# Kernel tuning notes

Hardware: AMD Instinct MI355X
Metric: run time of the kernel (lower is better)

## Reference

```python
import jax, jax.numpy as jnp
import numpy as np

IN_F = 128
OUT_F = 128
GROUPS = 8
NUM_F = 8
B = 16
NP_ = 4096


def setup_inputs() -> dict:
    key = jax.random.key(0)
    ks = jax.random.split(key, 6)
    x = jax.random.normal(ks[0], (B, NP_, IN_F), dtype=jnp.float32)
    grid = jnp.arange(NUM_F, dtype=jnp.float32) + 1.0                      # [num_f]
    base_weight = jax.random.normal(ks[1], (OUT_F, IN_F), dtype=jnp.float32) * 0.05
    scale_sp = jnp.ones((OUT_F,), dtype=jnp.float32)
    coef = jax.random.uniform(ks[2], (GROUPS, 1, NUM_F), dtype=jnp.float32)
    conv_w = jax.random.normal(ks[3], (NUM_F, OUT_F, IN_F), dtype=jnp.float32) * 0.05  # grouped 1x1 conv
    conv_b = jax.random.normal(ks[4], (NUM_F, OUT_F), dtype=jnp.float32) * 0.05
    return {"x": x, "grid": grid, "base_weight": base_weight,
            "scale_sp": scale_sp, "coef": coef, "conv_w": conv_w, "conv_b": conv_b}


def reference(x, grid, base_weight, scale_sp, coef, conv_w, conv_b):
    Bd, Nd, D = x.shape
    num_f = grid.shape[0]
    groups = coef.shape[0]
    gsz = D // groups
    xf = x.reshape(Bd * Nd, D)                                  # [batch, in]
    # base path: SiLU then linear (no bias)
    base = jax.nn.silu(xf) @ base_weight.T                       # [batch, out]
    # spline path: sin(grid * x), broadcast coef per (group, f)
    s = jnp.sin(grid[None, :, None] * xf[:, None, :])            # [batch, num_f, in]
    cm = coef[:, 0, :].T                                         # [num_f, groups]
    s = s.reshape(-1, num_f, groups, gsz) * cm[None, :, :, None]
    s = s.reshape(-1, num_f, D)                                  # [batch, num_f, in]
    # grouped 1x1 conv == per-f GEMM
    spline = jnp.einsum('bfi,foi->bfo', s, conv_w) + conv_b[None]
    spline = spline.sum(axis=1) * scale_sp                       # [batch, out]
    out = (base + spline).reshape(Bd, Nd, -1)
    return out
```

## Files before the change

### kernel.cpp

```cpp
#include <hip/hip_runtime.h>
#include <hip/hip_bf16.h>
#include <stdint.h>

#define IN_F   128
#define OUT_F  128
#define NUM_F  8
#define NROWS  (16*4096)

typedef __bf16  bf16x8  __attribute__((ext_vector_type(8)));
typedef float   f32x16  __attribute__((ext_vector_type(16)));
typedef float   f32x4   __attribute__((ext_vector_type(4)));

#define WP_CHUNKS (8*9*4*64)
#define SBLK      36864

__device__ __attribute__((aligned(256))) __bf16 g_Wp[WP_CHUNKS * 8];
__device__ float  g_bias[OUT_F];

__global__ __launch_bounds__(256) void skan_prep(
    const float* __restrict__ base_w,
    const float* __restrict__ scale,
    const float* __restrict__ coef,
    const float* __restrict__ conv_w,
    const float* __restrict__ conv_b)
{
    int gid = blockIdx.x * 256 + threadIdx.x;
    int l  = gid & 63;
    int t  = (gid >> 6) & 3;
    int r  = gid >> 8;
    int s  = r / 9;
    int fb = r % 9;
    int n  = t * 32 + (l & 31);
    int k0 = s * 16 + (l >> 5) * 8;
    __bf16* dst = g_Wp + (size_t)gid * 8;
    if (fb == 0) {
        #pragma unroll
        for (int j = 0; j < 8; ++j)
            dst[j] = (__bf16)base_w[n * IN_F + k0 + j];
    } else {
        int f = fb - 1;
        float sc = scale[n];
        #pragma unroll
        for (int j = 0; j < 8; ++j) {
            int k = k0 + j;
            float v = conv_w[((size_t)f * OUT_F + n) * IN_F + k]
                      * coef[(k >> 4) * NUM_F + f] * sc;
            dst[j] = (__bf16)v;
        }
    }
    if (gid < OUT_F) {
        float b = 0.f;
        #pragma unroll
        for (int f = 0; f < NUM_F; ++f) b += conv_b[f * OUT_F + gid];
        g_bias[gid] = b * scale[gid];
    }
}

__device__ __forceinline__ void gld_lds16(const void* g, void* l) {
    __builtin_amdgcn_global_load_lds(
        (const __attribute__((address_space(1))) uint32_t*)g,
        (__attribute__((address_space(3))) uint32_t*)l, 16, 0, 0);
}

__global__ __launch_bounds__(256, 2) void skan_main(
    const float* __restrict__ x,
    float* __restrict__ out)
{
    __shared__ uint4 smem4[4608];
    char* smem = (char*)smem4;

    const int tid = threadIdx.x;
    const int w   = tid >> 6;
    const int l   = tid & 63;
    const int hl  = l & 31;
    const int h   = l >> 5;
    const int m0  = blockIdx.x * 128 + w * 32;
    const int m   = m0 + hl;

    const char* wpb = (const char*)g_Wp;

    #pragma unroll
    for (int r = 0; r < 9; ++r)
        gld_lds16(wpb + (r * 256 + tid) * 16, smem + (r * 256 + tid) * 16);
    asm volatile("" ::: "memory");

    const f32x4* x4 = (const f32x4*)x + (size_t)m * (IN_F / 4) + 2 * h;
    f32x4 xa[8], xb[8];
    xa[0] = x4[0]; xb[0] = x4[1];
    xa[1] = x4[4]; xb[1] = x4[5];

    f32x16 acc[4];
    #pragma unroll
    for (int t = 0; t < 4; ++t)
        #pragma unroll
        for (int r = 0; r < 16; ++r) acc[t][r] = 0.f;

    #pragma unroll
    for (int s = 0; s < 8; ++s) {
        if (s < 7) asm volatile("s_waitcnt vmcnt(2)" ::: "memory");
        else       asm volatile("s_waitcnt vmcnt(0)" ::: "memory");
        __builtin_amdgcn_s_barrier();

        if (s < 7) {
            const char* src = wpb + (size_t)(s + 1) * SBLK;
            char*       dst = smem + ((s + 1) & 1) * SBLK;
            #pragma unroll
            for (int r = 0; r < 9; ++r)
                gld_lds16(src + (r * 256 + tid) * 16, dst + (r * 256 + tid) * 16);
        }
        asm volatile("" ::: "memory");
        if (s < 6) { xa[s + 2] = x4[4 * (s + 2)]; xb[s + 2] = x4[4 * (s + 2) + 1]; }

        bf16x8 af[9];
        #pragma unroll
        for (int j = 0; j < 8; ++j) {
            float v = (j < 4) ? xa[s][j] : xb[s][j - 4];
            float sv = v * __builtin_amdgcn_rcpf(1.0f + __expf(-v));
            af[0][j] = (__bf16)sv;
            float u  = __builtin_amdgcn_fractf(v * 0.15915494309189535f);
            float s1 = __builtin_amdgcn_sinf(u);
            float c2 = 2.0f * __builtin_amdgcn_cosf(u);
            af[1][j] = (__bf16)s1;
            float sp = s1;
            float sc = c2 * s1;
            af[2][j] = (__bf16)sc;
            #pragma unroll
            for (int f = 3; f <= 8; ++f) {
                float sn = c2 * sc - sp;
                af[f][j] = (__bf16)sn;
                sp = sc; sc = sn;
            }
        }

        const bf16x8* bp = (const bf16x8*)(smem + (s & 1) * SBLK);
        #pragma unroll
        for (int fb = 0; fb < 9; ++fb)
            #pragma unroll
            for (int t = 0; t < 4; ++t) {
                bf16x8 b = bp[(fb * 4 + t) * 64 + l];
                acc[t] = __builtin_amdgcn_mfma_f32_32x32x16_bf16(af[fb], b, acc[t], 0, 0, 0);
            }
    }

    #pragma unroll
    for (int t = 0; t < 4; ++t) {
        float bv = g_bias[t * 32 + hl];
        #pragma unroll
        for (int r = 0; r < 16; ++r) {
            int row = (r & 3) + 8 * (r >> 2) + 4 * h;
            out[(size_t)(m0 + row) * OUT_F + t * 32 + hl] = acc[t][r] + bv;
        }
    }
}

extern "C" void kernel_launch(void* const* d_in, const int* in_sizes, int n_in,
                              void* d_out, int out_size, void* d_ws, size_t ws_size,
                              hipStream_t stream) {
    const float* x      = (const float*)d_in[0];
    const float* base_w = (const float*)d_in[2];
    const float* scale  = (const float*)d_in[3];
    const float* coef   = (const float*)d_in[4];
    const float* conv_w = (const float*)d_in[5];
    const float* conv_b = (const float*)d_in[6];
    float* out = (float*)d_out;
    (void)d_ws; (void)ws_size;

    skan_prep<<<WP_CHUNKS / 256, 256, 0, stream>>>(base_w, scale, coef, conv_w, conv_b);
    skan_main<<<NROWS / 128, 256, 0, stream>>>(x, out);
}
```

Measured before the change: 109.0 us.

## Retile waves to 64x64 output blocks and double-buffer x loads

Each wave now computes a 64-row by 64-column output tile (2x2 MFMA tiles) instead of 32 rows by all 128 columns. It therefore loads only half of each B stage from LDS, and each B fragment feeds two MFMAs. In exchange, each wave computes silu/sin features for twice as many rows. Because the two column-half waves of a row pair compute identical features, the transcendental work per block doubles. The x prefetch is reduced to a two-slot ring issued after the feature computation, with the vmcnt wait adjusted to match.

Result: no change. 110.4 us (+1.3%).

```diff
diff --git a/kernel.cpp b/kernel.cpp
--- a/kernel.cpp
+++ b/kernel.cpp
@@ -62,6 +62,24 @@
         (__attribute__((address_space(3))) uint32_t*)l, 16, 0, 0);
 }
 
+__device__ __forceinline__ void skan_af(float v, bf16x8* af, int j) {
+    float sv = v * __builtin_amdgcn_rcpf(1.0f + __expf(-v));
+    af[0][j] = (__bf16)sv;
+    float u  = __builtin_amdgcn_fractf(v * 0.15915494309189535f);
+    float s1 = __builtin_amdgcn_sinf(u);
+    float c2 = 2.0f * __builtin_amdgcn_cosf(u);
+    af[1][j] = (__bf16)s1;
+    float sp = s1;
+    float sc = c2 * s1;
+    af[2][j] = (__bf16)sc;
+    #pragma unroll
+    for (int f = 3; f <= 8; ++f) {
+        float sn = c2 * sc - sp;
+        af[f][j] = (__bf16)sn;
+        sp = sc; sc = sn;
+    }
+}
+
 __global__ __launch_bounds__(256, 2) void skan_main(
     const float* __restrict__ x,
     float* __restrict__ out)
@@ -74,8 +92,10 @@
     const int l   = tid & 63;
     const int hl  = l & 31;
     const int h   = l >> 5;
-    const int m0  = blockIdx.x * 128 + w * 32;
-    const int m   = m0 + hl;
+    const int rw  = w >> 1;
+    const int cw  = w & 1;
+    const int mlo = blockIdx.x * 128 + rw * 64 + hl;
+    const int mhi = mlo + 32;
 
     const char* wpb = (const char*)g_Wp;
 
@@ -84,10 +104,11 @@
         gld_lds16(wpb + (r * 256 + tid) * 16, smem + (r * 256 + tid) * 16);
     asm volatile("" ::: "memory");
 
-    const f32x4* x4 = (const f32x4*)x + (size_t)m * (IN_F / 4) + 2 * h;
-    f32x4 xa[8], xb[8];
-    xa[0] = x4[0]; xb[0] = x4[1];
-    xa[1] = x4[4]; xb[1] = x4[5];
+    const f32x4* xLo = (const f32x4*)x + (size_t)mlo * (IN_F / 4) + 2 * h;
+    const f32x4* xHi = (const f32x4*)x + (size_t)mhi * (IN_F / 4) + 2 * h;
+    f32x4 xal[2], xbl[2], xah[2], xbh[2];
+    xal[0] = xLo[0]; xbl[0] = xLo[1]; xah[0] = xHi[0]; xbh[0] = xHi[1];
+    xal[1] = xLo[4]; xbl[1] = xLo[5]; xah[1] = xHi[4]; xbh[1] = xHi[5];
 
     f32x16 acc[4];
     #pragma unroll
@@ -97,7 +118,7 @@
 
     #pragma unroll
     for (int s = 0; s < 8; ++s) {
-        if (s < 7) asm volatile("s_waitcnt vmcnt(2)" ::: "memory");
+        if (s < 7) asm volatile("s_waitcnt vmcnt(4)" ::: "memory");
         else       asm volatile("s_waitcnt vmcnt(0)" ::: "memory");
         __builtin_amdgcn_s_barrier();
 
@@ -109,46 +130,44 @@
                 gld_lds16(src + (r * 256 + tid) * 16, dst + (r * 256 + tid) * 16);
         }
         asm volatile("" ::: "memory");
-        if (s < 6) { xa[s + 2] = x4[4 * (s + 2)]; xb[s + 2] = x4[4 * (s + 2) + 1]; }
 
-        bf16x8 af[9];
+        bf16x8 afl[9], afh[9];
         #pragma unroll
         for (int j = 0; j < 8; ++j) {
-            float v = (j < 4) ? xa[s][j] : xb[s][j - 4];
-            float sv = v * __builtin_amdgcn_rcpf(1.0f + __expf(-v));
-            af[0][j] = (__bf16)sv;
-            float u  = __builtin_amdgcn_fractf(v * 0.15915494309189535f);
-            float s1 = __builtin_amdgcn_sinf(u);
-            float c2 = 2.0f * __builtin_amdgcn_cosf(u);
-            af[1][j] = (__bf16)s1;
-            float sp = s1;
-            float sc = c2 * s1;
-            af[2][j] = (__bf16)sc;
-            #pragma unroll
-            for (int f = 3; f <= 8; ++f) {
-                float sn = c2 * sc - sp;
-                af[f][j] = (__bf16)sn;
-                sp = sc; sc = sn;
-            }
+            skan_af((j < 4) ? xal[s & 1][j] : xbl[s & 1][j - 4], afl, j);
+            skan_af((j < 4) ? xah[s & 1][j] : xbh[s & 1][j - 4], afh, j);
         }
+
+        if (s < 6) {
+            xal[s & 1] = xLo[4 * (s + 2)]; xbl[s & 1] = xLo[4 * (s + 2) + 1];
+            xah[s & 1] = xHi[4 * (s + 2)]; xbh[s & 1] = xHi[4 * (s + 2) + 1];
+        }
+        asm volatile("" ::: "memory");
 
         const bf16x8* bp = (const bf16x8*)(smem + (s & 1) * SBLK);
         #pragma unroll
-        for (int fb = 0; fb < 9; ++fb)
-            #pragma unroll
-            for (int t = 0; t < 4; ++t) {
-                bf16x8 b = bp[(fb * 4 + t) * 64 + l];
-                acc[t] = __builtin_amdgcn_mfma_f32_32x32x16_bf16(af[fb], b, acc[t], 0, 0, 0);
-            }
+        for (int fb = 0; fb < 9; ++fb) {
+            bf16x8 b0 = bp[(fb * 4 + 2 * cw) * 64 + l];
+            bf16x8 b1 = bp[(fb * 4 + 2 * cw + 1) * 64 + l];
+            acc[0] = __builtin_amdgcn_mfma_f32_32x32x16_bf16(afl[fb], b0, acc[0], 0, 0, 0);
+            acc[1] = __builtin_amdgcn_mfma_f32_32x32x16_bf16(afl[fb], b1, acc[1], 0, 0, 0);
+            acc[2] = __builtin_amdgcn_mfma_f32_32x32x16_bf16(afh[fb], b0, acc[2], 0, 0, 0);
+            acc[3] = __builtin_amdgcn_mfma_f32_32x32x16_bf16(afh[fb], b1, acc[3], 0, 0, 0);
+        }
     }
 
     #pragma unroll
-    for (int t = 0; t < 4; ++t) {
-        float bv = g_bias[t * 32 + hl];
+    for (int rt = 0; rt < 2; ++rt) {
+        int rowbase = blockIdx.x * 128 + rw * 64 + rt * 32;
         #pragma unroll
-        for (int r = 0; r < 16; ++r) {
-            int row = (r & 3) + 8 * (r >> 2) + 4 * h;
-            out[(size_t)(m0 + row) * OUT_F + t * 32 + hl] = acc[t][r] + bv;
+        for (int tc = 0; tc < 2; ++tc) {
+            int colbase = cw * 64 + tc * 32;
+            float bv = g_bias[colbase + hl];
+            #pragma unroll
+            for (int r = 0; r < 16; ++r) {
+                int row = rowbase + (r & 3) + 8 * (r >> 2) + 4 * h;
+                out[(size_t)row * OUT_F + colbase + hl] = acc[rt * 2 + tc][r] + bv;
+            }
         }
     }
 }
```
